# Kernel optimization log

Hardware: AMD Instinct MI355X
Metric: run time of the kernel (lower is better)

The kernel has to match this reference:

```python
import jax, jax.numpy as jnp
import numpy as np
import math

D = 768
H = 12
HD = D // H  # 64
B, N = 16, 1024
EPS = 1e-5


def _rope(x, cos, sin):
    # x: [B,N,H,hd]; cos,sin: [1,N,1,hd]
    x1, x2 = x[..., ::2], x[..., 1::2]
    return jnp.concatenate(
        [x1 * cos[..., ::2] - x2 * sin[..., ::2],
         x1 * sin[..., 1::2] + x2 * cos[..., 1::2]], axis=-1)


def setup_inputs() -> dict:
    key = jax.random.key(0)
    ks = jax.random.split(key, 8)
    s = 1.0 / math.sqrt(D)  # xavier-ish scale
    return {
        "x": jax.random.normal(ks[0], (B, N, D), jnp.float32),
        "rope_emb": jax.random.normal(ks[1], (N, HD), jnp.float32),
        "ln_w": jnp.ones((D,), jnp.float32),
        "ln_b": jnp.zeros((D,), jnp.float32),
        "enc_w": jax.random.normal(ks[2], (D, D), jnp.float32) * s,
        "enc_b": jnp.zeros((D,), jnp.float32),
        "qk_w": jax.random.normal(ks[3], (D, D), jnp.float32) * s,
        "qk_b": jnp.zeros((D,), jnp.float32),
        "v_w": jax.random.normal(ks[4], (D, D), jnp.float32) * s,
        "v_b": jnp.zeros((D,), jnp.float32),
        "out_w": jax.random.normal(ks[5], (D, D), jnp.float32) * s,
        "out_b": jnp.zeros((D,), jnp.float32),
        "gate_w": jax.random.normal(ks[6], (D, D), jnp.float32) * s,
        "gate_b": jnp.zeros((D,), jnp.float32),
    }


def reference(x, rope_emb, ln_w, ln_b, enc_w, enc_b, qk_w, qk_b,
              v_w, v_b, out_w, out_b, gate_w, gate_b):
    b, n, d = x.shape
    # Pre-LayerNorm
    mu = jnp.mean(x, axis=-1, keepdims=True)
    var = jnp.mean(jnp.square(x - mu), axis=-1, keepdims=True)
    x_norm = (x - mu) / jnp.sqrt(var + EPS) * ln_w + ln_b
    # sparse latent encoder
    x_latent = jax.nn.relu(x_norm @ enc_w.T + enc_b)
    qk = (x_latent @ qk_w.T + qk_b).reshape(b, n, H, HD)
    v = (x_latent @ v_w.T + v_b).reshape(b, n, H, HD)
    ang = rope_emb[:, :HD]
    cos = jnp.cos(ang)[None, :, None, :]
    sin = jnp.sin(ang)[None, :, None, :]
    qk = _rope(qk, cos, sin)
    # raw (softmax-free) attention, Q=K
    scores = jnp.einsum('bnhd,bmhd->bhnm', qk, qk) / math.sqrt(HD)
    attn = jnp.einsum('bhnm,bmhd->bnhd', scores, v).reshape(b, n, d)
    attn = attn @ out_w.T + out_b
    gate = jax.nn.sigmoid(x_norm @ gate_w.T + gate_b)
    return x + gate * attn
```

## Files before the change

### kernel.cpp

```cpp
#include <hip/hip_runtime.h>

typedef __bf16 bf16;
typedef __bf16 bf16x4 __attribute__((ext_vector_type(4)));
typedef __bf16 bf16x8 __attribute__((ext_vector_type(8)));
typedef float floatx4 __attribute__((ext_vector_type(4)));

#define DD 768
#define NH 12
#define HDIM 64
#define BB 16
#define NN 1024
#define MTOT (BB*NN)
#define WELEM (DD*DD)

__device__ __forceinline__ void async_cp16(const void* g, void* l) {
  __builtin_amdgcn_global_load_lds((const __attribute__((address_space(1))) void*)g,
                                   (__attribute__((address_space(3))) void*)l, 16, 0, 0);
}

__global__ __launch_bounds__(256) void ln_kernel(const float* __restrict__ x,
    const float* __restrict__ w, const float* __restrict__ b, bf16* __restrict__ A) {
  int row = blockIdx.x * 4 + (threadIdx.x >> 6);
  int lane = threadIdx.x & 63;
  const float4* xr = (const float4*)(x + (size_t)row * DD);
  float4 v[3];
  float s = 0.f;
#pragma unroll
  for (int i = 0; i < 3; i++) {
    v[i] = xr[lane + 64 * i];
    s += v[i].x + v[i].y + v[i].z + v[i].w;
  }
#pragma unroll
  for (int o = 32; o; o >>= 1) s += __shfl_xor(s, o);
  float mu = s * (1.f / 768.f);
  float vs = 0.f;
#pragma unroll
  for (int i = 0; i < 3; i++) {
    float dx;
    dx = v[i].x - mu; vs += dx * dx;
    dx = v[i].y - mu; vs += dx * dx;
    dx = v[i].z - mu; vs += dx * dx;
    dx = v[i].w - mu; vs += dx * dx;
  }
#pragma unroll
  for (int o = 32; o; o >>= 1) vs += __shfl_xor(vs, o);
  float rstd = rsqrtf(vs * (1.f / 768.f) + 1e-5f);
  const float4* wv = (const float4*)w;
  const float4* bv = (const float4*)b;
  bf16* Ar = A + (size_t)row * DD;
#pragma unroll
  for (int i = 0; i < 3; i++) {
    int c4 = lane + 64 * i;
    float4 ww = wv[c4], bb = bv[c4];
    bf16x4 pk;
    pk[0] = (bf16)((v[i].x - mu) * rstd * ww.x + bb.x);
    pk[1] = (bf16)((v[i].y - mu) * rstd * ww.y + bb.y);
    pk[2] = (bf16)((v[i].z - mu) * rstd * ww.z + bb.z);
    pk[3] = (bf16)((v[i].w - mu) * rstd * ww.w + bb.w);
    *(bf16x4*)(Ar + c4 * 4) = pk;
  }
}

__global__ __launch_bounds__(256) void convw_kernel(const float* __restrict__ w0,
    const float* __restrict__ w1, const float* __restrict__ w2,
    const float* __restrict__ w3, const float* __restrict__ w4, bf16* __restrict__ out) {
  int i = blockIdx.x * 256 + threadIdx.x;
  int which = i / (WELEM / 4);
  int off = (i % (WELEM / 4)) * 4;
  const float* s = which == 0 ? w0 : which == 1 ? w1 : which == 2 ? w2 : which == 3 ? w3 : w4;
  float4 v = *(const float4*)(s + off);
  bf16x4 pk;
  pk[0] = (bf16)v.x; pk[1] = (bf16)v.y; pk[2] = (bf16)v.z; pk[3] = (bf16)v.w;
  *(bf16x4*)(out + (size_t)i * 4) = pk;
}

template<int EPI>
__global__ __launch_bounds__(256) void gemm_kernel(
    const bf16* __restrict__ Aop, const bf16* __restrict__ W,
    const float* __restrict__ bias,
    bf16* __restrict__ Cb, float* __restrict__ Cf,
    const float* __restrict__ Xres, const bf16* __restrict__ Gate) {
  __shared__ bf16 As[128 * 32];
  __shared__ bf16 Bs[128 * 32];
  int tid = threadIdx.x;
  int wave = tid >> 6, lane = tid & 63;
  int quad = lane >> 4, l16 = lane & 15;
  int wm = wave & 1, wn = wave >> 1;
  int bn = blockIdx.x, bm = blockIdx.y;
  int srow = lane >> 2, scol = (lane & 3) * 8;

  const bf16* Ag = Aop + (size_t)(bm * 128 + srow) * DD + scol;
  const bf16* Bg = W + (size_t)(bn * 128 + srow) * DD + scol;

  floatx4 acc[4][4];
#pragma unroll
  for (int i = 0; i < 4; i++)
#pragma unroll
    for (int j = 0; j < 4; j++)
      acc[i][j] = (floatx4){0.f, 0.f, 0.f, 0.f};

  for (int k0 = 0; k0 < DD; k0 += 32) {
    __syncthreads();
#pragma unroll
    for (int it = 0; it < 2; it++) {
      int r0 = (it * 4 + wave) * 16;
      async_cp16(Ag + (size_t)r0 * DD + k0, &As[r0 * 32]);
      async_cp16(Bg + (size_t)r0 * DD + k0, &Bs[r0 * 32]);
    }
    __syncthreads();
    bf16x8 a[4], b[4];
#pragma unroll
    for (int i = 0; i < 4; i++) a[i] = *(const bf16x8*)&As[(wm * 64 + i * 16 + l16) * 32 + quad * 8];
#pragma unroll
    for (int i = 0; i < 4; i++) b[i] = *(const bf16x8*)&Bs[(wn * 64 + i * 16 + l16) * 32 + quad * 8];
#pragma unroll
    for (int mi = 0; mi < 4; mi++)
#pragma unroll
      for (int ni = 0; ni < 4; ni++)
        acc[mi][ni] = __builtin_amdgcn_mfma_f32_16x16x32_bf16(a[mi], b[ni], acc[mi][ni], 0, 0, 0);
  }

#pragma unroll
  for (int ni = 0; ni < 4; ni++) {
    int gc = bn * 128 + wn * 64 + ni * 16 + l16;
    float bz = bias[gc];
#pragma unroll
    for (int mi = 0; mi < 4; mi++) {
      int gm0 = bm * 128 + wm * 64 + mi * 16 + quad * 4;
      if (EPI == 2) {
        int h = gc >> 6, dd2 = gc & 63;
        int b_ = gm0 >> 10, n0 = gm0 & 1023;
        bf16x4 pk;
#pragma unroll
        for (int r = 0; r < 4; r++) pk[r] = (bf16)(acc[mi][ni][r] + bz);
        *(bf16x4*)&Cb[(((size_t)b_ * NH + h) * HDIM + dd2) * NN + n0] = pk;
      } else {
#pragma unroll
        for (int r = 0; r < 4; r++) {
          float v = acc[mi][ni][r] + bz;
          size_t idx = (size_t)(gm0 + r) * DD + gc;
          if (EPI == 0) Cb[idx] = (bf16)fmaxf(v, 0.f);
          else if (EPI == 1) Cb[idx] = (bf16)v;
          else if (EPI == 3) Cb[idx] = (bf16)(1.f / (1.f + __expf(-v)));
          else { float g = (float)Gate[idx]; Cf[idx] = Xres[idx] + g * v; }
        }
      }
    }
  }
}

__global__ __launch_bounds__(256) void rope_kernel(const bf16* __restrict__ QKraw,
    const float* __restrict__ rope, bf16* __restrict__ QKr, bf16* __restrict__ QKrT) {
  int blk = blockIdx.x;
  int bh = blk >> 7;
  int nc = blk & 127;
  int b_ = bh / NH, h_ = bh % NH;
  int t = threadIdx.x;
  int noff = t >> 5;
  int d = t & 31;
  int n = nc * 8 + noff;
  size_t ibase = ((size_t)(b_ * NN + n)) * DD + h_ * HDIM;
  float x1 = (float)QKraw[ibase + 2 * d];
  float x2 = (float)QKraw[ibase + 2 * d + 1];
  float a0 = rope[n * HDIM + 2 * d];
  float a1 = rope[n * HDIM + 2 * d + 1];
  float o1 = x1 * __cosf(a0) - x2 * __sinf(a0);
  float o2 = x1 * __sinf(a1) + x2 * __cosf(a1);
  size_t obase = ((size_t)(b_ * NN + n)) * DD + h_ * HDIM;
  QKr[obase + d] = (bf16)o1;
  QKr[obase + 32 + d] = (bf16)o2;
  size_t tbase = ((size_t)bh * HDIM + d) * NN + n;
  QKrT[tbase] = (bf16)o1;
  QKrT[tbase + (size_t)32 * NN] = (bf16)o2;
}

__global__ __launch_bounds__(256) void attn_kernel(const bf16* __restrict__ QKr,
    const bf16* __restrict__ QKrT, const bf16* __restrict__ VT, bf16* __restrict__ attn) {
  __shared__ float Tp[64][64];
  __shared__ bf16 Tbf[64][72];
  int bh = blockIdx.x;
  int tid = threadIdx.x, wave = tid >> 6, lane = tid & 63;
  int quad = lane >> 4, l16 = lane & 15;
  const bf16* Qt = QKrT + (size_t)bh * (HDIM * NN);
  const bf16* Vt = VT + (size_t)bh * (HDIM * NN);

  floatx4 acc[4][4];
#pragma unroll
  for (int i = 0; i < 4; i++)
#pragma unroll
    for (int j = 0; j < 4; j++)
      acc[i][j] = (floatx4){0.f, 0.f, 0.f, 0.f};

  int kbase = wave * 256;
#pragma unroll
  for (int k0 = 0; k0 < 256; k0 += 32) {
    bf16x8 a[4], b[4];
#pragma unroll
    for (int i = 0; i < 4; i++) a[i] = *(const bf16x8*)&Qt[(size_t)(i * 16 + l16) * NN + kbase + k0 + quad * 8];
#pragma unroll
    for (int i = 0; i < 4; i++) b[i] = *(const bf16x8*)&Vt[(size_t)(i * 16 + l16) * NN + kbase + k0 + quad * 8];
#pragma unroll
    for (int mi = 0; mi < 4; mi++)
#pragma unroll
      for (int ni = 0; ni < 4; ni++)
        acc[mi][ni] = __builtin_amdgcn_mfma_f32_16x16x32_bf16(a[mi], b[ni], acc[mi][ni], 0, 0, 0);
  }
#pragma unroll
  for (int w = 0; w < 4; w++) {
    if (wave == w) {
#pragma unroll
      for (int mi = 0; mi < 4; mi++)
#pragma unroll
        for (int ni = 0; ni < 4; ni++)
#pragma unroll
          for (int r = 0; r < 4; r++) {
            float val = acc[mi][ni][r];
            float* p = &Tp[mi * 16 + quad * 4 + r][ni * 16 + l16];
            if (w == 0) *p = val; else *p += val;
          }
    }
    __syncthreads();
  }
  for (int e = tid; e < 4096; e += 256) {
    int d1 = e >> 6, d2 = e & 63;
    Tbf[d2][d1] = (bf16)(Tp[d1][d2] * 0.125f);
  }
  __syncthreads();

  int b_ = bh / NH, h_ = bh % NH;
  const bf16* Q = QKr + (size_t)(b_ * NN) * DD + h_ * HDIM;
  bf16* Ao = attn + (size_t)(b_ * NN) * DD + h_ * HDIM;
  bf16x8 Bf[4][2];
#pragma unroll
  for (int ni = 0; ni < 4; ni++)
#pragma unroll
    for (int ks = 0; ks < 2; ks++)
      Bf[ni][ks] = *(const bf16x8*)&Tbf[ni * 16 + l16][ks * 32 + quad * 8];

  for (int mi = 0; mi < 16; mi++) {
    int nrow = wave * 256 + mi * 16;
    bf16x8 a0 = *(const bf16x8*)&Q[(size_t)(nrow + l16) * DD + quad * 8];
    bf16x8 a1 = *(const bf16x8*)&Q[(size_t)(nrow + l16) * DD + 32 + quad * 8];
    floatx4 o[4];
#pragma unroll
    for (int ni = 0; ni < 4; ni++) o[ni] = (floatx4){0.f, 0.f, 0.f, 0.f};
#pragma unroll
    for (int ni = 0; ni < 4; ni++) {
      o[ni] = __builtin_amdgcn_mfma_f32_16x16x32_bf16(a0, Bf[ni][0], o[ni], 0, 0, 0);
      o[ni] = __builtin_amdgcn_mfma_f32_16x16x32_bf16(a1, Bf[ni][1], o[ni], 0, 0, 0);
    }
#pragma unroll
    for (int ni = 0; ni < 4; ni++)
#pragma unroll
      for (int r = 0; r < 4; r++)
        Ao[(size_t)(nrow + quad * 4 + r) * DD + ni * 16 + l16] = (bf16)o[ni][r];
  }
}

extern "C" void kernel_launch(void* const* d_in, const int* in_sizes, int n_in,
                              void* d_out, int out_size, void* d_ws, size_t ws_size,
                              hipStream_t stream) {
  const float* x      = (const float*)d_in[0];
  const float* rope   = (const float*)d_in[1];
  const float* ln_w   = (const float*)d_in[2];
  const float* ln_b   = (const float*)d_in[3];
  const float* enc_w  = (const float*)d_in[4];
  const float* enc_b  = (const float*)d_in[5];
  const float* qk_w   = (const float*)d_in[6];
  const float* qk_b   = (const float*)d_in[7];
  const float* v_w    = (const float*)d_in[8];
  const float* v_b    = (const float*)d_in[9];
  const float* out_w  = (const float*)d_in[10];
  const float* out_b  = (const float*)d_in[11];
  const float* gate_w = (const float*)d_in[12];
  const float* gate_b = (const float*)d_in[13];

  char* w = (char*)d_ws;
  const size_t S = (size_t)MTOT * DD * 2;
  bf16* A     = (bf16*)(w);
  bf16* L     = (bf16*)(w + S);
  bf16* QKraw = (bf16*)(w + 2 * S);
  bf16* QKr   = (bf16*)(w + 3 * S);
  bf16* QKrT  = (bf16*)(w + 4 * S);
  bf16* VT    = (bf16*)(w + 5 * S);
  bf16* Wb    = (bf16*)(w + 6 * S);
  bf16* Gate  = QKraw;
  bf16* attnb = L;

  ln_kernel<<<dim3(MTOT / 4), dim3(256), 0, stream>>>(x, ln_w, ln_b, A);
  convw_kernel<<<dim3(5 * WELEM / 4 / 256), dim3(256), 0, stream>>>(enc_w, qk_w, v_w, out_w, gate_w, Wb);

  dim3 ggrid(DD / 128, MTOT / 128);
  gemm_kernel<0><<<ggrid, dim3(256), 0, stream>>>(A, Wb + 0 * (size_t)WELEM, enc_b, L, nullptr, nullptr, nullptr);
  gemm_kernel<1><<<ggrid, dim3(256), 0, stream>>>(L, Wb + 1 * (size_t)WELEM, qk_b, QKraw, nullptr, nullptr, nullptr);
  rope_kernel<<<dim3(BB * NH * 128), dim3(256), 0, stream>>>(QKraw, rope, QKr, QKrT);
  gemm_kernel<2><<<ggrid, dim3(256), 0, stream>>>(L, Wb + 2 * (size_t)WELEM, v_b, VT, nullptr, nullptr, nullptr);
  gemm_kernel<3><<<ggrid, dim3(256), 0, stream>>>(A, Wb + 4 * (size_t)WELEM, gate_b, Gate, nullptr, nullptr, nullptr);
  attn_kernel<<<dim3(BB * NH), dim3(256), 0, stream>>>(QKr, QKrT, VT, attnb);
  gemm_kernel<4><<<ggrid, dim3(256), 0, stream>>>(attnb, Wb + 3 * (size_t)WELEM, out_b, nullptr, (float*)d_out, x, Gate);
}
```

Before: 389.0 us.

## Merge paired GEMMs sharing an input, remap blocks per XCD, vectorize epilogues

Concatenates the enc and gate weights, and the qk and v weights, so that two GEMMs sharing the same A operand each run as one 1536-block launch. This removes two launches and lets A tiles be reused. Blocks are remapped so each XCD handles a contiguous band of row tiles, which should improve L2 locality of A. For the non-transposed outputs, the MFMA operands are swapped so each lane holds four consecutive columns, allowing float4 bias loads and vectorized bf16x4/float4 stores in place of scalar stores. Workspace buffers are reassigned to match the fused outputs.

```diff
diff --git a/kernel.cpp b/kernel.cpp
--- a/kernel.cpp
+++ b/kernel.cpp
@@ -75,18 +75,17 @@
 }
 
 template<int EPI>
-__global__ __launch_bounds__(256) void gemm_kernel(
+__device__ __forceinline__ void gemm_body(
+    int bm, int bn, int bnl,
     const bf16* __restrict__ Aop, const bf16* __restrict__ W,
     const float* __restrict__ bias,
     bf16* __restrict__ Cb, float* __restrict__ Cf,
-    const float* __restrict__ Xres, const bf16* __restrict__ Gate) {
-  __shared__ bf16 As[128 * 32];
-  __shared__ bf16 Bs[128 * 32];
+    const float* __restrict__ Xres, const bf16* __restrict__ Gate,
+    bf16* As, bf16* Bs) {
   int tid = threadIdx.x;
   int wave = tid >> 6, lane = tid & 63;
   int quad = lane >> 4, l16 = lane & 15;
   int wm = wave & 1, wn = wave >> 1;
-  int bn = blockIdx.x, bm = blockIdx.y;
   int srow = lane >> 2, scol = (lane & 3) * 8;
 
   const bf16* Ag = Aop + (size_t)(bm * 128 + srow) * DD + scol;
@@ -113,39 +112,95 @@
     for (int i = 0; i < 4; i++) a[i] = *(const bf16x8*)&As[(wm * 64 + i * 16 + l16) * 32 + quad * 8];
 #pragma unroll
     for (int i = 0; i < 4; i++) b[i] = *(const bf16x8*)&Bs[(wn * 64 + i * 16 + l16) * 32 + quad * 8];
-#pragma unroll
-    for (int mi = 0; mi < 4; mi++)
-#pragma unroll
-      for (int ni = 0; ni < 4; ni++)
-        acc[mi][ni] = __builtin_amdgcn_mfma_f32_16x16x32_bf16(a[mi], b[ni], acc[mi][ni], 0, 0, 0);
-  }
-
-#pragma unroll
-  for (int ni = 0; ni < 4; ni++) {
-    int gc = bn * 128 + wn * 64 + ni * 16 + l16;
-    float bz = bias[gc];
-#pragma unroll
-    for (int mi = 0; mi < 4; mi++) {
-      int gm0 = bm * 128 + wm * 64 + mi * 16 + quad * 4;
-      if (EPI == 2) {
-        int h = gc >> 6, dd2 = gc & 63;
+    if (EPI == 2) {
+#pragma unroll
+      for (int mi = 0; mi < 4; mi++)
+#pragma unroll
+        for (int ni = 0; ni < 4; ni++)
+          acc[mi][ni] = __builtin_amdgcn_mfma_f32_16x16x32_bf16(a[mi], b[ni], acc[mi][ni], 0, 0, 0);
+    } else {
+#pragma unroll
+      for (int mi = 0; mi < 4; mi++)
+#pragma unroll
+        for (int ni = 0; ni < 4; ni++)
+          acc[mi][ni] = __builtin_amdgcn_mfma_f32_16x16x32_bf16(b[ni], a[mi], acc[mi][ni], 0, 0, 0);
+    }
+  }
+
+  if (EPI == 2) {
+#pragma unroll
+    for (int ni = 0; ni < 4; ni++) {
+      int gc = bnl * 128 + wn * 64 + ni * 16 + l16;
+      float bz = bias[gc];
+      int h = gc >> 6, dd2 = gc & 63;
+#pragma unroll
+      for (int mi = 0; mi < 4; mi++) {
+        int gm0 = bm * 128 + wm * 64 + mi * 16 + quad * 4;
         int b_ = gm0 >> 10, n0 = gm0 & 1023;
         bf16x4 pk;
 #pragma unroll
         for (int r = 0; r < 4; r++) pk[r] = (bf16)(acc[mi][ni][r] + bz);
         *(bf16x4*)&Cb[(((size_t)b_ * NH + h) * HDIM + dd2) * NN + n0] = pk;
-      } else {
-#pragma unroll
-        for (int r = 0; r < 4; r++) {
-          float v = acc[mi][ni][r] + bz;
-          size_t idx = (size_t)(gm0 + r) * DD + gc;
-          if (EPI == 0) Cb[idx] = (bf16)fmaxf(v, 0.f);
-          else if (EPI == 1) Cb[idx] = (bf16)v;
-          else if (EPI == 3) Cb[idx] = (bf16)(1.f / (1.f + __expf(-v)));
-          else { float g = (float)Gate[idx]; Cf[idx] = Xres[idx] + g * v; }
+      }
+    }
+  } else {
+#pragma unroll
+    for (int mi = 0; mi < 4; mi++) {
+      int gm = bm * 128 + wm * 64 + mi * 16 + l16;
+#pragma unroll
+      for (int ni = 0; ni < 4; ni++) {
+        int gc = bnl * 128 + wn * 64 + ni * 16 + quad * 4;
+        float4 bz = *(const float4*)&bias[gc];
+        float v0 = acc[mi][ni][0] + bz.x;
+        float v1 = acc[mi][ni][1] + bz.y;
+        float v2 = acc[mi][ni][2] + bz.z;
+        float v3 = acc[mi][ni][3] + bz.w;
+        size_t idx = (size_t)gm * DD + gc;
+        if (EPI == 4) {
+          bf16x4 g = *(const bf16x4*)&Gate[idx];
+          float4 xr = *(const float4*)&Xres[idx];
+          float4 o;
+          o.x = xr.x + (float)g[0] * v0;
+          o.y = xr.y + (float)g[1] * v1;
+          o.z = xr.z + (float)g[2] * v2;
+          o.w = xr.w + (float)g[3] * v3;
+          *(float4*)&Cf[idx] = o;
+        } else {
+          bf16x4 pk;
+          if (EPI == 0) {
+            pk[0] = (bf16)fmaxf(v0, 0.f); pk[1] = (bf16)fmaxf(v1, 0.f);
+            pk[2] = (bf16)fmaxf(v2, 0.f); pk[3] = (bf16)fmaxf(v3, 0.f);
+          } else if (EPI == 1) {
+            pk[0] = (bf16)v0; pk[1] = (bf16)v1; pk[2] = (bf16)v2; pk[3] = (bf16)v3;
+          } else {
+            pk[0] = (bf16)(1.f / (1.f + __expf(-v0)));
+            pk[1] = (bf16)(1.f / (1.f + __expf(-v1)));
+            pk[2] = (bf16)(1.f / (1.f + __expf(-v2)));
+            pk[3] = (bf16)(1.f / (1.f + __expf(-v3)));
+          }
+          *(bf16x4*)&Cb[idx] = pk;
         }
       }
     }
+  }
+}
+
+template<int EPI_LO, int EPI_HI, int NBN>
+__global__ __launch_bounds__(256) void gemm_kernel(
+    const bf16* __restrict__ Aop, const bf16* __restrict__ W,
+    const float* __restrict__ bias_lo, const float* __restrict__ bias_hi,
+    bf16* __restrict__ C_lo, bf16* __restrict__ C_hi, float* __restrict__ Cf,
+    const float* __restrict__ Xres, const bf16* __restrict__ Gate) {
+  __shared__ bf16 As[128 * 32];
+  __shared__ bf16 Bs[128 * 32];
+  int blk = blockIdx.x;
+  int xcd = blk & 7, slot = blk >> 3;
+  int bm = xcd * 16 + slot / NBN;
+  int bn = slot % NBN;
+  if (NBN == 12 && bn >= 6) {
+    gemm_body<EPI_HI>(bm, bn, bn - 6, Aop, W, bias_hi, C_hi, Cf, Xres, Gate, As, Bs);
+  } else {
+    gemm_body<EPI_LO>(bm, bn, bn, Aop, W, bias_lo, C_lo, Cf, Xres, Gate, As, Bs);
   }
 }
 
@@ -277,25 +332,32 @@
 
   char* w = (char*)d_ws;
   const size_t S = (size_t)MTOT * DD * 2;
-  bf16* A     = (bf16*)(w);
-  bf16* L     = (bf16*)(w + S);
-  bf16* QKraw = (bf16*)(w + 2 * S);
-  bf16* QKr   = (bf16*)(w + 3 * S);
-  bf16* QKrT  = (bf16*)(w + 4 * S);
-  bf16* VT    = (bf16*)(w + 5 * S);
-  bf16* Wb    = (bf16*)(w + 6 * S);
-  bf16* Gate  = QKraw;
-  bf16* attnb = L;
+  bf16* s0 = (bf16*)(w);
+  bf16* s1 = (bf16*)(w + S);
+  bf16* s2 = (bf16*)(w + 2 * S);
+  bf16* s3 = (bf16*)(w + 3 * S);
+  bf16* s4 = (bf16*)(w + 4 * S);
+  bf16* s5 = (bf16*)(w + 5 * S);
+  bf16* Wb = (bf16*)(w + 6 * S);
+
+  bf16* A = s0;
+  bf16* L = s1;
+  bf16* Gate = s2;
+  bf16* QKraw = s0;
+  bf16* QKr = s3;
+  bf16* QKrT = s4;
+  bf16* VT = s5;
+  bf16* attnb = s1;
 
   ln_kernel<<<dim3(MTOT / 4), dim3(256), 0, stream>>>(x, ln_w, ln_b, A);
-  convw_kernel<<<dim3(5 * WELEM / 4 / 256), dim3(256), 0, stream>>>(enc_w, qk_w, v_w, out_w, gate_w, Wb);
-
-  dim3 ggrid(DD / 128, MTOT / 128);
-  gemm_kernel<0><<<ggrid, dim3(256), 0, stream>>>(A, Wb + 0 * (size_t)WELEM, enc_b, L, nullptr, nullptr, nullptr);
-  gemm_kernel<1><<<ggrid, dim3(256), 0, stream>>>(L, Wb + 1 * (size_t)WELEM, qk_b, QKraw, nullptr, nullptr, nullptr);
+  convw_kernel<<<dim3(5 * WELEM / 4 / 256), dim3(256), 0, stream>>>(enc_w, gate_w, qk_w, v_w, out_w, Wb);
+
+  gemm_kernel<0, 3, 12><<<dim3(1536), dim3(256), 0, stream>>>(
+      A, Wb, enc_b, gate_b, L, Gate, nullptr, nullptr, nullptr);
+  gemm_kernel<1, 2, 12><<<dim3(1536), dim3(256), 0, stream>>>(
+      L, Wb + 2 * (size_t)WELEM, qk_b, v_b, QKraw, VT, nullptr, nullptr, nullptr);
   rope_kernel<<<dim3(BB * NH * 128), dim3(256), 0, stream>>>(QKraw, rope, QKr, QKrT);
-  gemm_kernel<2><<<ggrid, dim3(256), 0, stream>>>(L, Wb + 2 * (size_t)WELEM, v_b, VT, nullptr, nullptr, nullptr);
-  gemm_kernel<3><<<ggrid, dim3(256), 0, stream>>>(A, Wb + 4 * (size_t)WELEM, gate_b, Gate, nullptr, nullptr, nullptr);
   attn_kernel<<<dim3(BB * NH), dim3(256), 0, stream>>>(QKr, QKrT, VT, attnb);
-  gemm_kernel<4><<<ggrid, dim3(256), 0, stream>>>(attnb, Wb + 3 * (size_t)WELEM, out_b, nullptr, (float*)d_out, x, Gate);
-}
+  gemm_kernel<4, 4, 6><<<dim3(768), dim3(256), 0, stream>>>(
+      attnb, Wb + 4 * (size_t)WELEM, out_b, nullptr, nullptr, nullptr, (float*)d_out, x, Gate);
+}
```

Result: faster. 360.0 us (-7.5%).
